# Kernel optimization log

Measured on AMD Instinct MI355X. Metric: run time of the kernel, lower is better.

The kernel has to match this reference:

```python
import jax, jax.numpy as jnp
import numpy as np

B, T, I, H, G = 64, 512, 512, 512, 5  # batch, seq, input, hidden, gates (f,i,o,u,k)


def setup_inputs() -> dict:
    key = jax.random.key(0)
    ks = jax.random.split(key, 9)
    s_in = 1.0 / np.sqrt(I)
    s_h = 1.0 / np.sqrt(H)
    inp = {"x": jax.random.normal(ks[0], (B, T, I), dtype=jnp.float32)}
    # stacked Linear weights, torch layout [out, in]: y = x @ W.T + b
    inp["Wx_f"] = jax.random.uniform(ks[1], (G, H, I), jnp.float32, -s_in, s_in)
    inp["bx_f"] = jax.random.uniform(ks[2], (G, H), jnp.float32, -s_in, s_in)
    inp["Wh_f"] = jax.random.uniform(ks[3], (G, H, H), jnp.float32, -s_h, s_h)
    inp["bh_f"] = jax.random.uniform(ks[4], (G, H), jnp.float32, -s_h, s_h)
    inp["Wx_b"] = jax.random.uniform(ks[5], (G, H, I), jnp.float32, -s_in, s_in)
    inp["bx_b"] = jax.random.uniform(ks[6], (G, H), jnp.float32, -s_in, s_in)
    inp["Wh_b"] = jax.random.uniform(ks[7], (G, H, H), jnp.float32, -s_h, s_h)
    inp["bh_b"] = jax.random.uniform(ks[8], (G, H), jnp.float32, -s_h, s_h)
    return inp


def _run_direction(x, Wx, bx, Wh, bh):
    b, t, _ = x.shape
    h_dim = Wx.shape[1]
    # Precompute all input projections once: [T, B, G, H]
    xp = jnp.einsum('bti,ghi->tbgh', x, Wx) + bx

    def step(carry, xp_t):
        h, k, kp = carry
        g = xp_t + jnp.einsum('bi,goi->bgo', h, Wh) + bh  # [B, G, H]
        f = jax.nn.sigmoid(g[:, 0])
        i = jax.nn.sigmoid(g[:, 1])
        o = jax.nn.sigmoid(g[:, 2])
        u = jax.nn.sigmoid(g[:, 3])
        kp_new = u * jnp.tanh(g[:, 4]) + (1.0 - u) * kp
        k_new = f * k + i * kp_new
        h_new = o * jnp.tanh(k_new)
        return (h_new, k_new, kp_new), h_new

    z = jnp.zeros((b, h_dim), x.dtype)
    _, hs = jax.lax.scan(step, (z, z, z), xp)  # hs: [T, B, H]
    return jnp.transpose(hs, (1, 0, 2))  # [B, T, H]


def reference(x, Wx_f, bx_f, Wh_f, bh_f, Wx_b, bx_b, Wh_b, bh_b):
    out_f = _run_direction(x, Wx_f, bx_f, Wh_f, bh_f)
    out_b = _run_direction(x[:, ::-1], Wx_b, bx_b, Wh_b, bh_b)[:, ::-1]
    # dropout_rate=0.0 / eval mode -> Dropout is identity
    return jnp.concatenate([out_f, out_b], axis=2)  # [B, T, 2H]
```

## Files before the change

kernel.cpp:

```cpp
#include <hip/hip_runtime.h>
#include <hip/hip_bf16.h>

#define B_   64
#define T_   512
#define I_   512
#define H_   512
#define G_   5
#define NROW 2560
#define KD   512

typedef __attribute__((ext_vector_type(8))) __bf16 bf16x8;
typedef __attribute__((ext_vector_type(4))) float  f32x4;
typedef __attribute__((ext_vector_type(2))) unsigned long long u64x2;
typedef unsigned long long u64;

#define MFMA16(A, Bf, C) __builtin_amdgcn_mfma_f32_16x16x32_bf16(A, Bf, C, 0, 0, 0)

__device__ __forceinline__ unsigned short f2bf(float f) {
  unsigned u = __builtin_bit_cast(unsigned, f);
  u = (u + 0x7fffu + ((u >> 16) & 1u)) >> 16;
  return (unsigned short)u;
}
__device__ __forceinline__ float bf2f(unsigned short s) {
  unsigned u = ((unsigned)s) << 16;
  return __builtin_bit_cast(float, u);
}
__device__ __forceinline__ float sigm(float x) { return 1.f / (1.f + __expf(-x)); }
__device__ __forceinline__ float tanh_fast(float x) {
  return 1.f - 2.f / (__expf(2.f * x) + 1.f);
}
__device__ __forceinline__ u64 al64(const u64* p) {
  return __hip_atomic_load(p, __ATOMIC_RELAXED, __HIP_MEMORY_SCOPE_AGENT);
}
__device__ __forceinline__ void as64(u64* p, u64 v) {
  __hip_atomic_store(p, v, __ATOMIC_RELAXED, __HIP_MEMORY_SCOPE_AGENT);
}
__device__ __forceinline__ unsigned al32(const unsigned* p) {
  return __hip_atomic_load(p, __ATOMIC_RELAXED, __HIP_MEMORY_SCOPE_AGENT);
}
__device__ __forceinline__ void st32(unsigned* p, unsigned v) {
  __hip_atomic_store(p, v, __ATOMIC_RELAXED, __HIP_MEMORY_SCOPE_AGENT);
}

#define OFF_XP   ((size_t)0)
#define OFF_XB   ((size_t)335544320)
#define OFF_W2X  ((size_t)369098752)
#define OFF_W2H  ((size_t)374341632)
#define OFF_BIAS ((size_t)379584512)
#define OFF_HB   ((size_t)379604992)
#define OFF_BAR  ((size_t)379867136)
#define WS_NEED  ((size_t)379871232)

__global__ void k_sentinel(float* out, int n) {
  int i = blockIdx.x * 256 + threadIdx.x;
  if (i < n) out[i] = 10000.0f;
}

__global__ void k_cvt_weights(const float* __restrict__ Wx_f, const float* __restrict__ Wh_f,
                              const float* __restrict__ Wx_b, const float* __restrict__ Wh_b,
                              const float* __restrict__ bx_f, const float* __restrict__ bh_f,
                              const float* __restrict__ bx_b, const float* __restrict__ bh_b,
                              unsigned short* __restrict__ W2x, unsigned short* __restrict__ W2h,
                              float* __restrict__ bias2) {
  int idx = blockIdx.x * 256 + threadIdx.x;
  int dir = idx / (NROW * KD);
  int r   = idx % (NROW * KD);
  W2x[idx] = f2bf(dir ? Wx_b[r] : Wx_f[r]);
  W2h[idx] = f2bf(dir ? Wh_b[r] : Wh_f[r]);
  if (idx < 2 * NROW) {
    int d2 = idx / NROW, n = idx % NROW;
    bias2[idx] = d2 ? (bx_b[n] + bh_b[n]) : (bx_f[n] + bh_f[n]);
  }
}

__global__ void k_cvt_x(const float* __restrict__ x, unsigned short* __restrict__ xb) {
  int idx = blockIdx.x * 256 + threadIdx.x;
  xb[idx] = f2bf(x[idx]);
}

__global__ void k_zero_h(unsigned short* __restrict__ hb, unsigned* __restrict__ bar) {
  int idx = blockIdx.x * 256 + threadIdx.x;
  hb[idx] = 0;
  if (idx < 1024) bar[idx] = 0;
}

__global__ __launch_bounds__(256) void k_gemm_xp(
    const unsigned short* __restrict__ W2x,
    const unsigned short* __restrict__ xb,
    const float* __restrict__ bias2,
    unsigned short* __restrict__ xp)
{
  const int tid = threadIdx.x;
  const int lane = tid & 63, wv = tid >> 6;
  int bz = blockIdx.x;
  const int dir = bz / (20 * 256); bz %= (20 * 256);
  const int nblk = bz / 256, mblk = bz % 256;
  const int n0 = nblk * 128, m0 = mblk * 128;
  const int l15 = lane & 15, l4 = lane >> 4;
  const int nh = wv >> 1, mh = wv & 1;

  __shared__ unsigned short Al[128 * 72];
  __shared__ unsigned short Bl[128 * 72];

  const unsigned short* Wd = W2x + (size_t)dir * NROW * KD;

  f32x4 acc[4][4];
  f32x4 zz = {0.f, 0.f, 0.f, 0.f};
#pragma unroll
  for (int i = 0; i < 4; ++i)
#pragma unroll
    for (int j = 0; j < 4; ++j) acc[i][j] = zz;

  for (int k0 = 0; k0 < KD; k0 += 64) {
#pragma unroll
    for (int j = 0; j < 4; ++j) {
      int sg = j * 256 + tid;
      int row = sg >> 3, ko = (sg & 7) * 8;
      bf16x8 va = *(const bf16x8*)(Wd + (size_t)(n0 + row) * KD + k0 + ko);
      *(bf16x8*)(Al + row * 72 + ko) = va;
      int m = m0 + row;
      int ss = m >> 6, b = m & 63;
      int trow = dir ? (T_ - 1 - ss) : ss;
      bf16x8 vb = *(const bf16x8*)(xb + ((size_t)b * T_ + trow) * I_ + k0 + ko);
      *(bf16x8*)(Bl + row * 72 + ko) = vb;
    }
    __syncthreads();
#pragma unroll
    for (int kk = 0; kk < 2; ++kk) {
      bf16x8 af[4], bfr[4];
#pragma unroll
      for (int f = 0; f < 4; ++f) {
        af[f]  = *(const bf16x8*)(Al + (nh * 64 + f * 16 + l15) * 72 + kk * 32 + l4 * 8);
        bfr[f] = *(const bf16x8*)(Bl + (mh * 64 + f * 16 + l15) * 72 + kk * 32 + l4 * 8);
      }
#pragma unroll
      for (int fi = 0; fi < 4; ++fi)
#pragma unroll
        for (int fj = 0; fj < 4; ++fj)
          acc[fi][fj] = MFMA16(af[fi], bfr[fj], acc[fi][fj]);
    }
    __syncthreads();
  }

#pragma unroll
  for (int fi = 0; fi < 4; ++fi) {
#pragma unroll
    for (int fj = 0; fj < 4; ++fj) {
#pragma unroll
      for (int r = 0; r < 4; ++r) {
        int n = n0 + nh * 64 + fi * 16 + l4 * 4 + r;
        int m = m0 + mh * 64 + fj * 16 + l15;
        int ss = m >> 6, b = m & 63;
        float v = acc[fi][fj][r] + bias2[dir * NROW + n];
        xp[(((size_t)dir * T_ + ss) * NROW + n) * 64 + b] = f2bf(v);
      }
    }
  }
}

#define GSTEP(CUR, NXT, NT, NP)                                            \
  {                                                                        \
    _Pragma("unroll")                                                      \
    for (int ks = 0; ks < 16; ++ks)                                        \
      NXT[ks] = *(const bf16x8*)(w_lds + ((NP)*16 + l15) * 520 + ks * 32 + l4 * 8); \
    _Pragma("unroll")                                                      \
    for (int ks = 0; ks < 16; ++ks) {                                      \
      u64x2 t2 = {lo[ks], hi[ks]};                                         \
      bf16x8 a = __builtin_bit_cast(bf16x8, t2);                           \
      acc[NT] = MFMA16(a, CUR[ks], acc[NT]);                               \
    }                                                                      \
  }

__global__ __launch_bounds__(128, 1) void k_recurrent(
    const unsigned short* __restrict__ W2h,
    const unsigned short* __restrict__ xp,
    unsigned short* __restrict__ hbuf,
    float* __restrict__ out,
    unsigned* __restrict__ bar)
{
  const int tid = threadIdx.x;
  const int lane = tid & 63, w = tid >> 6;
  const int bid = blockIdx.x;
  const int dir = bid & 1, bhalf = (bid >> 1) & 1, ublk = bid >> 2;
  const int l15 = lane & 15, l4 = lane >> 4;

  __shared__ unsigned short w_lds[80 * 520];
  __shared__ float          g_sh[2][16 * 84];
  __shared__ unsigned short x_sh[2][80 * 18];

  for (int it = 0; it < 40; ++it) {
    int seg = it * 128 + tid;
    int r = seg >> 6, c8 = seg & 63;
    const unsigned short* src =
        W2h + ((size_t)dir * NROW + (r >> 4) * H_ + ublk * 16 + (r & 15)) * KD + c8 * 8;
    *(bf16x8*)(w_lds + r * 520 + c8 * 8) = *(const bf16x8*)src;
  }
  __syncthreads();

  float* gl = g_sh[w];
  unsigned short* xl = x_sh[w];

  const unsigned short* xpd = xp + (size_t)dir * T_ * NROW * 64;
  const int xoff = bhalf * 16 + w * 8;
  const int batch0 = bhalf * 32 + w * 16;

  unsigned* fl = bar + (dir * 2 + bhalf) * 64;
  const int myflag = ublk * 2 + w;

  const unsigned short* hc = hbuf + (size_t)dir * B_ * H_;
  unsigned short*       hn = hbuf + (size_t)(2 + dir) * B_ * H_;

  const int bl = lane >> 2, uq = (lane & 3) * 4;
  float kst[4] = {0.f, 0.f, 0.f, 0.f}, kp[4] = {0.f, 0.f, 0.f, 0.f};

  unsigned xr[10];
  auto ld_xp = [&](int s) {
    const unsigned* xb32 = (const unsigned*)(xpd + (size_t)s * NROW * 64);
#pragma unroll
    for (int j = 0; j < 10; ++j) {
      int id = j * 64 + lane;
      int r = id >> 3, c = id & 7;
      xr[j] = xb32[((size_t)(r >> 4) * H_ + ublk * 16 + (r & 15)) * 32 + xoff + c];
    }
  };
  ld_xp(0);

  f32x4 zz = {0.f, 0.f, 0.f, 0.f};
  bf16x8 wfA[16], wfB[16];
#pragma unroll
  for (int ks = 0; ks < 16; ++ks)
    wfA[ks] = *(const bf16x8*)(w_lds + l15 * 520 + ks * 32 + l4 * 8);

  auto body = [&](int s, bf16x8 (&cw)[16], bf16x8 (&nw)[16]) {
    if (s) {
      __builtin_amdgcn_sched_barrier(0);
      unsigned tgt = (unsigned)s;
      for (;;) {
        unsigned v = al32(fl + (lane & 31) * 2 + w);
        if (!__any(v < tgt)) break;
        __builtin_amdgcn_s_sleep(1);
      }
      __builtin_amdgcn_sched_barrier(0);
    }

#pragma unroll
    for (int j = 0; j < 10; ++j) {
      int id = j * 64 + lane;
      int r = id >> 3, c = id & 7;
      *(unsigned*)(xl + r * 18 + c * 2) = xr[j];
    }

    const u64* hq = (const u64*)hc;
    u64 lo[16], hi[16];
#pragma unroll
    for (int ks = 0; ks < 16; ++ks) {
      size_t ci = (size_t)(batch0 + l15) * 128 + ks * 8 + l4 * 2;
      lo[ks] = al64(hq + ci);
      hi[ks] = al64(hq + ci + 1);
    }

    f32x4 acc[5] = {zz, zz, zz, zz, zz};
    GSTEP(cw, nw, 0, 1)
    GSTEP(nw, cw, 1, 2)
    GSTEP(cw, nw, 2, 3)
    GSTEP(nw, cw, 3, 4)
    GSTEP(cw, nw, 4, 0)

#pragma unroll
    for (int Nt = 0; Nt < 5; ++Nt)
#pragma unroll
      for (int rr = 0; rr < 4; ++rr)
        gl[(l4 * 4 + rr) * 84 + Nt * 16 + l15] = acc[Nt][rr];
    asm volatile("s_waitcnt lgkmcnt(0)" ::: "memory");
    __builtin_amdgcn_sched_barrier(0);

    float hv[4];
#pragma unroll
    for (int j = 0; j < 4; ++j) {
      int u = uq + j;
      float g0 = gl[bl * 84 + 0 * 16 + u] + bf2f(xl[(0 * 16 + u) * 18 + bl]);
      float g1 = gl[bl * 84 + 1 * 16 + u] + bf2f(xl[(1 * 16 + u) * 18 + bl]);
      float g2 = gl[bl * 84 + 2 * 16 + u] + bf2f(xl[(2 * 16 + u) * 18 + bl]);
      float g3 = gl[bl * 84 + 3 * 16 + u] + bf2f(xl[(3 * 16 + u) * 18 + bl]);
      float g4 = gl[bl * 84 + 4 * 16 + u] + bf2f(xl[(4 * 16 + u) * 18 + bl]);
      float ff = sigm(g0), ii = sigm(g1), oo = sigm(g2), uu = sigm(g3), tk = tanh_fast(g4);
      kp[j]  = uu * tk + (1.f - uu) * kp[j];
      kst[j] = ff * kst[j] + ii * kp[j];
      hv[j]  = oo * tanh_fast(kst[j]);
    }

    u64 hw = (u64)f2bf(hv[0]) | ((u64)f2bf(hv[1]) << 16) |
             ((u64)f2bf(hv[2]) << 32) | ((u64)f2bf(hv[3]) << 48);
    as64((u64*)hn + (size_t)(batch0 + bl) * 128 + (ublk * 16 + uq) / 4, hw);

    int tout = dir ? (T_ - 1 - s) : s;
    float4 o4 = {hv[0], hv[1], hv[2], hv[3]};
    if (s + 1 < T_) {
      asm volatile("s_waitcnt vmcnt(0)" ::: "memory");
      st32(&fl[myflag], (unsigned)(s + 1));
      *(float4*)&out[((size_t)(batch0 + bl) * T_ + tout) * (2 * H_) +
                     dir * H_ + ublk * 16 + uq] = o4;
      ld_xp(s + 1);
    } else {
      *(float4*)&out[((size_t)(batch0 + bl) * T_ + tout) * (2 * H_) +
                     dir * H_ + ublk * 16 + uq] = o4;
    }

    const unsigned short* tp = hc; hc = hn; hn = (unsigned short*)tp;
  };

  for (int s = 0; s < T_; s += 2) {
    body(s,     wfA, wfB);
    body(s + 1, wfB, wfA);
  }
}

extern "C" void kernel_launch(void* const* d_in, const int* in_sizes, int n_in,
                              void* d_out, int out_size, void* d_ws, size_t ws_size,
                              hipStream_t stream) {
  const float* x    = (const float*)d_in[0];
  const float* Wx_f = (const float*)d_in[1];
  const float* bx_f = (const float*)d_in[2];
  const float* Wh_f = (const float*)d_in[3];
  const float* bh_f = (const float*)d_in[4];
  const float* Wx_b = (const float*)d_in[5];
  const float* bx_b = (const float*)d_in[6];
  const float* Wh_b = (const float*)d_in[7];
  const float* bh_b = (const float*)d_in[8];
  float* out = (float*)d_out;

  if (ws_size < WS_NEED) {
    k_sentinel<<<(out_size + 255) / 256, 256, 0, stream>>>(out, out_size);
    return;
  }

  char* ws = (char*)d_ws;
  unsigned short* xp    = (unsigned short*)(ws + OFF_XP);
  unsigned short* xb    = (unsigned short*)(ws + OFF_XB);
  unsigned short* W2x   = (unsigned short*)(ws + OFF_W2X);
  unsigned short* W2h   = (unsigned short*)(ws + OFF_W2H);
  float*          bias2 = (float*)(ws + OFF_BIAS);
  unsigned short* hbuf  = (unsigned short*)(ws + OFF_HB);
  unsigned*       bar   = (unsigned*)(ws + OFF_BAR);

  k_cvt_weights<<<(2 * NROW * KD) / 256, 256, 0, stream>>>(
      Wx_f, Wh_f, Wx_b, Wh_b, bx_f, bh_f, bx_b, bh_b, W2x, W2h, bias2);
  k_cvt_x<<<(B_ * T_ * I_) / 256, 256, 0, stream>>>(x, xb);
  k_zero_h<<<(2 * 2 * B_ * H_) / 256, 256, 0, stream>>>(hbuf, bar);
  k_gemm_xp<<<2 * 20 * 256, 256, 0, stream>>>(W2x, xb, bias2, xp);
  k_recurrent<<<128, 128, 0, stream>>>(W2h, xp, hbuf, out, bar);
}
```

Measured before the change: 2.553 ms.

## Group recurrent workgroups by XCD and sync via XCD-local L2 flags

The recurrent kernel now launches 256 single-wave workgroups instead of 128 two-wave ones. Each workgroup reads its XCD id and takes a rank within that XCD, so each of the 8 (direction, batch-quarter) domains runs entirely on one XCD. Hidden-state exchange and step flags then go through per-domain buffers with sc0 loads and stores, aiming to keep the per-step handoff inside the local L2 instead of going to device-coherent memory. A mirrored device-scope copy of h and the flags serves as a fallback if the placement is uneven or the spin times out. The cost is double writes of h and flags, an extra startup barrier, and reliance on workgroups being spread evenly across XCDs.

```diff
diff --git a/kernel.cpp b/kernel.cpp
--- a/kernel.cpp
+++ b/kernel.cpp
@@ -49,7 +49,8 @@
 #define OFF_BIAS ((size_t)379584512)
 #define OFF_HB   ((size_t)379604992)
 #define OFF_BAR  ((size_t)379867136)
-#define WS_NEED  ((size_t)379871232)
+#define OFF_HMIR ((size_t)379871232)
+#define WS_NEED  ((size_t)380133376)
 
 __global__ void k_sentinel(float* out, int n) {
   int i = blockIdx.x * 256 + threadIdx.x;
@@ -78,9 +79,11 @@
   xb[idx] = f2bf(x[idx]);
 }
 
-__global__ void k_zero_h(unsigned short* __restrict__ hb, unsigned* __restrict__ bar) {
+__global__ void k_zero_h(unsigned* __restrict__ h2, unsigned* __restrict__ hm,
+                         unsigned* __restrict__ bar) {
   int idx = blockIdx.x * 256 + threadIdx.x;
-  hb[idx] = 0;
+  h2[idx] = 0;
+  hm[idx] = 0;
   if (idx < 1024) bar[idx] = 0;
 }
 
@@ -164,63 +167,69 @@
     for (int ks = 0; ks < 16; ++ks)                                        \
       NXT[ks] = *(const bf16x8*)(w_lds + ((NP)*16 + l15) * 520 + ks * 32 + l4 * 8); \
     _Pragma("unroll")                                                      \
-    for (int ks = 0; ks < 16; ++ks) {                                      \
-      u64x2 t2 = {lo[ks], hi[ks]};                                         \
-      bf16x8 a = __builtin_bit_cast(bf16x8, t2);                           \
-      acc[NT] = MFMA16(a, CUR[ks], acc[NT]);                               \
-    }                                                                      \
-  }
-
-__global__ __launch_bounds__(128, 1) void k_recurrent(
+    for (int ks = 0; ks < 16; ++ks)                                        \
+      acc[NT] = MFMA16(ha[ks], CUR[ks], acc[NT]);                          \
+  }
+
+__global__ __launch_bounds__(64, 1) void k_recurrent(
     const unsigned short* __restrict__ W2h,
     const unsigned short* __restrict__ xp,
-    unsigned short* __restrict__ hbuf,
+    unsigned short* __restrict__ hb2,
+    unsigned short* __restrict__ hbm,
     float* __restrict__ out,
     unsigned* __restrict__ bar)
 {
-  const int tid = threadIdx.x;
-  const int lane = tid & 63, w = tid >> 6;
-  const int bid = blockIdx.x;
-  const int dir = bid & 1, bhalf = (bid >> 1) & 1, ublk = bid >> 2;
+  const int lane = threadIdx.x;
   const int l15 = lane & 15, l4 = lane >> 4;
 
   __shared__ unsigned short w_lds[80 * 520];
-  __shared__ float          g_sh[2][16 * 84];
-  __shared__ unsigned short x_sh[2][80 * 18];
-
-  for (int it = 0; it < 40; ++it) {
-    int seg = it * 128 + tid;
+  __shared__ float          gl[16 * 84];
+  __shared__ unsigned short xl[80 * 18];
+
+  unsigned xcd;
+  asm("s_getreg_b32 %0, hwreg(HW_REG_XCC_ID, 0, 4)" : "=s"(xcd));
+  xcd &= 7;
+  unsigned rank = 0;
+  if (lane == 0) rank = atomicAdd(&bar[512 + xcd], 1u);
+  rank = (unsigned)__shfl((int)rank, 0);
+  if (lane == 0) atomicAdd(&bar[520], 1u);
+  while (al32(&bar[520]) < 256u) __builtin_amdgcn_s_sleep(2);
+  bool good = true;
+#pragma unroll
+  for (int x = 0; x < 8; ++x) good = good && (al32(&bar[512 + x]) == 32u);
+
+  int dom, rk;
+  bool l3;
+  if (good && rank < 32u) { dom = (int)xcd; rk = (int)rank; l3 = false; }
+  else                    { dom = blockIdx.x >> 5; rk = blockIdx.x & 31; l3 = true; }
+
+  const int dir = dom >> 2, bq = dom & 3;
+
+  for (int it = 0; it < 80; ++it) {
+    int seg = it * 64 + lane;
     int r = seg >> 6, c8 = seg & 63;
     const unsigned short* src =
-        W2h + ((size_t)dir * NROW + (r >> 4) * H_ + ublk * 16 + (r & 15)) * KD + c8 * 8;
+        W2h + ((size_t)dir * NROW + (r >> 4) * H_ + rk * 16 + (r & 15)) * KD + c8 * 8;
     *(bf16x8*)(w_lds + r * 520 + c8 * 8) = *(const bf16x8*)src;
   }
-  __syncthreads();
-
-  float* gl = g_sh[w];
-  unsigned short* xl = x_sh[w];
 
   const unsigned short* xpd = xp + (size_t)dir * T_ * NROW * 64;
-  const int xoff = bhalf * 16 + w * 8;
-  const int batch0 = bhalf * 32 + w * 16;
-
-  unsigned* fl = bar + (dir * 2 + bhalf) * 64;
-  const int myflag = ublk * 2 + w;
-
-  const unsigned short* hc = hbuf + (size_t)dir * B_ * H_;
-  unsigned short*       hn = hbuf + (size_t)(2 + dir) * B_ * H_;
+  unsigned short* h2d = hb2 + (size_t)dom * 16384;
+  unsigned short* hmd = hbm + (size_t)dom * 16384;
+  unsigned* fl2 = bar + dom * 32;
+  unsigned* flm = bar + 256 + dom * 32;
 
   const int bl = lane >> 2, uq = (lane & 3) * 4;
   float kst[4] = {0.f, 0.f, 0.f, 0.f}, kp[4] = {0.f, 0.f, 0.f, 0.f};
 
   unsigned xr[10];
   auto ld_xp = [&](int s) {
-    const unsigned* xb32 = (const unsigned*)(xpd + (size_t)s * NROW * 64);
+    const unsigned* x32 = (const unsigned*)(xpd + (size_t)s * NROW * 64);
 #pragma unroll
     for (int j = 0; j < 10; ++j) {
       int id = j * 64 + lane;
-      int r = id >> 3, c = id & 7;
-      xr[j] = xb32[((size_t)(r >> 4) * H_ + ublk * 16 + (r & 15)) * 32 + xoff + c];
+      int rl = id >> 3, c = id & 7;
+      xr[j] = x32[((size_t)(rl >> 4) * H_ + rk * 16 + (rl & 15)) * 32 + bq * 8 + c];
     }
   };
   ld_xp(0);
@@ -235,28 +244,54 @@
     if (s) {
       __builtin_amdgcn_sched_barrier(0);
       unsigned tgt = (unsigned)s;
-      for (;;) {
-        unsigned v = al32(fl + (lane & 31) * 2 + w);
-        if (!__any(v < tgt)) break;
-        __builtin_amdgcn_s_sleep(1);
+      if (!l3) {
+        int spins = 0;
+        for (;;) {
+          unsigned v;
+          asm volatile("global_load_dword %0, %1, off sc0\n\ts_waitcnt vmcnt(0)"
+                       : "=v"(v) : "v"(fl2 + (lane & 31)) : "memory");
+          if (!__any(v < tgt)) break;
+          if (++spins > 16384) { l3 = true; break; }
+          __builtin_amdgcn_s_sleep(1);
+        }
+      }
+      if (l3) {
+        for (;;) {
+          unsigned v = al32(flm + (lane & 31));
+          if (!__any(v < tgt)) break;
+          __builtin_amdgcn_s_sleep(1);
+        }
       }
       __builtin_amdgcn_sched_barrier(0);
+    }
+
+    bf16x8 ha[16];
+    {
+      const unsigned short* hq =
+          (l3 ? hmd : h2d) + (s & 1) * 8192 + l15 * 512 + l4 * 8;
+      if (!l3) {
+#pragma unroll
+        for (int ks = 0; ks < 16; ++ks)
+          asm volatile("global_load_dwordx4 %0, %1, off sc0"
+                       : "=v"(ha[ks]) : "v"(hq + ks * 32));
+        asm volatile("s_waitcnt vmcnt(0)" ::: "memory");
+        __builtin_amdgcn_sched_barrier(0);
+      } else {
+#pragma unroll
+        for (int ks = 0; ks < 16; ++ks) {
+          u64 lo = al64((const u64*)(hq + ks * 32));
+          u64 hi = al64((const u64*)(hq + ks * 32) + 1);
+          u64x2 t2 = {lo, hi};
+          ha[ks] = __builtin_bit_cast(bf16x8, t2);
+        }
+      }
     }
 
 #pragma unroll
     for (int j = 0; j < 10; ++j) {
       int id = j * 64 + lane;
-      int r = id >> 3, c = id & 7;
-      *(unsigned*)(xl + r * 18 + c * 2) = xr[j];
-    }
-
-    const u64* hq = (const u64*)hc;
-    u64 lo[16], hi[16];
-#pragma unroll
-    for (int ks = 0; ks < 16; ++ks) {
-      size_t ci = (size_t)(batch0 + l15) * 128 + ks * 8 + l4 * 2;
-      lo[ks] = al64(hq + ci);
-      hi[ks] = al64(hq + ci + 1);
+      int rl = id >> 3, c = id & 7;
+      *(unsigned*)(xl + rl * 18 + c * 2) = xr[j];
     }
 
     f32x4 acc[5] = {zz, zz, zz, zz, zz};
@@ -291,22 +326,30 @@
 
     u64 hw = (u64)f2bf(hv[0]) | ((u64)f2bf(hv[1]) << 16) |
              ((u64)f2bf(hv[2]) << 32) | ((u64)f2bf(hv[3]) << 48);
-    as64((u64*)hn + (size_t)(batch0 + bl) * 128 + (ublk * 16 + uq) / 4, hw);
+    {
+      size_t off = (size_t)((s + 1) & 1) * 8192 + bl * 512 + rk * 16 + uq;
+      asm volatile("global_store_dwordx2 %0, %1, off"
+                   :: "v"(h2d + off), "v"(hw) : "memory");
+      as64((u64*)(hmd + off), hw);
+    }
 
     int tout = dir ? (T_ - 1 - s) : s;
     float4 o4 = {hv[0], hv[1], hv[2], hv[3]};
     if (s + 1 < T_) {
       asm volatile("s_waitcnt vmcnt(0)" ::: "memory");
-      st32(&fl[myflag], (unsigned)(s + 1));
-      *(float4*)&out[((size_t)(batch0 + bl) * T_ + tout) * (2 * H_) +
-                     dir * H_ + ublk * 16 + uq] = o4;
+      if (lane == 0) {
+        unsigned nf = (unsigned)(s + 1);
+        asm volatile("global_store_dword %0, %1, off"
+                     :: "v"(fl2 + rk), "v"(nf) : "memory");
+        st32(flm + rk, nf);
+      }
+      *(float4*)&out[((size_t)(bq * 16 + bl) * T_ + tout) * (2 * H_) +
+                     dir * H_ + rk * 16 + uq] = o4;
       ld_xp(s + 1);
     } else {
-      *(float4*)&out[((size_t)(batch0 + bl) * T_ + tout) * (2 * H_) +
-                     dir * H_ + ublk * 16 + uq] = o4;
-    }
-
-    const unsigned short* tp = hc; hc = hn; hn = (unsigned short*)tp;
+      *(float4*)&out[((size_t)(bq * 16 + bl) * T_ + tout) * (2 * H_) +
+                     dir * H_ + rk * 16 + uq] = o4;
+    }
   };
 
   for (int s = 0; s < T_; s += 2) {
@@ -340,13 +383,14 @@
   unsigned short* W2x   = (unsigned short*)(ws + OFF_W2X);
   unsigned short* W2h   = (unsigned short*)(ws + OFF_W2H);
   float*          bias2 = (float*)(ws + OFF_BIAS);
-  unsigned short* hbuf  = (unsigned short*)(ws + OFF_HB);
+  unsigned short* hb2   = (unsigned short*)(ws + OFF_HB);
   unsigned*       bar   = (unsigned*)(ws + OFF_BAR);
+  unsigned short* hbm   = (unsigned short*)(ws + OFF_HMIR);
 
   k_cvt_weights<<<(2 * NROW * KD) / 256, 256, 0, stream>>>(
       Wx_f, Wh_f, Wx_b, Wh_b, bx_f, bh_f, bx_b, bh_b, W2x, W2h, bias2);
   k_cvt_x<<<(B_ * T_ * I_) / 256, 256, 0, stream>>>(x, xb);
-  k_zero_h<<<(2 * 2 * B_ * H_) / 256, 256, 0, stream>>>(hbuf, bar);
+  k_zero_h<<<256, 256, 0, stream>>>((unsigned*)hb2, (unsigned*)hbm, bar);
   k_gemm_xp<<<2 * 20 * 256, 256, 0, stream>>>(W2x, xb, bias2, xp);
-  k_recurrent<<<128, 128, 0, stream>>>(W2h, xp, hbuf, out, bar);
-}
+  k_recurrent<<<256, 64, 0, stream>>>(W2h, xp, hb2, hbm, out, bar);
+}
```

Result: slower. 3.840 ms (+50.4%).

## Halve recurrent grid; each wave processes two batch sets per step to hide sync latency

Applied to the files above, without the earlier changes.

The recurrent kernel now launches 64 blocks instead of 128. Each wave handles two 16-batch sets in sequence within every timestep, with separate cell state, prefetched projections and barrier flags for each set. The aim is to overlap one set's barrier wait and global latency with the other set's compute, and to reduce the number of blocks taking part in each cross-block flag barrier. In exchange, each block does twice the serial work per step, and the per-set flag layout uses 32 blocks per group.

```diff
diff --git a/kernel.cpp b/kernel.cpp
--- a/kernel.cpp
+++ b/kernel.cpp
@@ -181,7 +181,7 @@
   const int tid = threadIdx.x;
   const int lane = tid & 63, w = tid >> 6;
   const int bid = blockIdx.x;
-  const int dir = bid & 1, bhalf = (bid >> 1) & 1, ublk = bid >> 2;
+  const int dir = bid & 1, ublk = bid >> 1;
   const int l15 = lane & 15, l4 = lane >> 4;
 
   __shared__ unsigned short w_lds[80 * 520];
@@ -201,29 +201,27 @@
   unsigned short* xl = x_sh[w];
 
   const unsigned short* xpd = xp + (size_t)dir * T_ * NROW * 64;
-  const int xoff = bhalf * 16 + w * 8;
-  const int batch0 = bhalf * 32 + w * 16;
-
-  unsigned* fl = bar + (dir * 2 + bhalf) * 64;
-  const int myflag = ublk * 2 + w;
+  const int setA = 2 * w, setB = 2 * w + 1;
 
   const unsigned short* hc = hbuf + (size_t)dir * B_ * H_;
   unsigned short*       hn = hbuf + (size_t)(2 + dir) * B_ * H_;
 
   const int bl = lane >> 2, uq = (lane & 3) * 4;
-  float kst[4] = {0.f, 0.f, 0.f, 0.f}, kp[4] = {0.f, 0.f, 0.f, 0.f};
-
-  unsigned xr[10];
-  auto ld_xp = [&](int s) {
+  float kstA[4] = {0.f, 0.f, 0.f, 0.f}, kpA[4] = {0.f, 0.f, 0.f, 0.f};
+  float kstB[4] = {0.f, 0.f, 0.f, 0.f}, kpB[4] = {0.f, 0.f, 0.f, 0.f};
+
+  unsigned xrA[10], xrB[10];
+  auto ld_xp = [&](int s, int set, unsigned (&xr)[10]) {
     const unsigned* xb32 = (const unsigned*)(xpd + (size_t)s * NROW * 64);
 #pragma unroll
     for (int j = 0; j < 10; ++j) {
       int id = j * 64 + lane;
       int r = id >> 3, c = id & 7;
-      xr[j] = xb32[((size_t)(r >> 4) * H_ + ublk * 16 + (r & 15)) * 32 + xoff + c];
+      xr[j] = xb32[((size_t)(r >> 4) * H_ + ublk * 16 + (r & 15)) * 32 + set * 8 + c];
     }
   };
-  ld_xp(0);
+  ld_xp(0, setA, xrA);
+  ld_xp(0, setB, xrB);
 
   f32x4 zz = {0.f, 0.f, 0.f, 0.f};
   bf16x8 wfA[16], wfB[16];
@@ -231,12 +229,17 @@
   for (int ks = 0; ks < 16; ++ks)
     wfA[ks] = *(const bf16x8*)(w_lds + l15 * 520 + ks * 32 + l4 * 8);
 
-  auto body = [&](int s, bf16x8 (&cw)[16], bf16x8 (&nw)[16]) {
+  auto body = [&](int s, int set, unsigned (&xr)[10],
+                  float (&kst)[4], float (&kp)[4],
+                  bf16x8 (&cw)[16], bf16x8 (&nw)[16]) {
+    unsigned* fl = bar + (dir * 4 + set) * 32;
+    const int batch0 = set * 16;
+
     if (s) {
       __builtin_amdgcn_sched_barrier(0);
       unsigned tgt = (unsigned)s;
       for (;;) {
-        unsigned v = al32(fl + (lane & 31) * 2 + w);
+        unsigned v = al32(fl + (lane & 31));
         if (!__any(v < tgt)) break;
         __builtin_amdgcn_s_sleep(1);
       }
@@ -297,21 +300,20 @@
     float4 o4 = {hv[0], hv[1], hv[2], hv[3]};
     if (s + 1 < T_) {
       asm volatile("s_waitcnt vmcnt(0)" ::: "memory");
-      st32(&fl[myflag], (unsigned)(s + 1));
+      if (lane == 0) st32(&fl[ublk], (unsigned)(s + 1));
       *(float4*)&out[((size_t)(batch0 + bl) * T_ + tout) * (2 * H_) +
                      dir * H_ + ublk * 16 + uq] = o4;
-      ld_xp(s + 1);
+      ld_xp(s + 1, set, xr);
     } else {
       *(float4*)&out[((size_t)(batch0 + bl) * T_ + tout) * (2 * H_) +
                      dir * H_ + ublk * 16 + uq] = o4;
     }
-
+  };
+
+  for (int s = 0; s < T_; ++s) {
+    body(s, setA, xrA, kstA, kpA, wfA, wfB);
+    body(s, setB, xrB, kstB, kpB, wfB, wfA);
     const unsigned short* tp = hc; hc = hn; hn = (unsigned short*)tp;
-  };
-
-  for (int s = 0; s < T_; s += 2) {
-    body(s,     wfA, wfB);
-    body(s + 1, wfB, wfA);
   }
 }
 
@@ -348,5 +350,5 @@
   k_cvt_x<<<(B_ * T_ * I_) / 256, 256, 0, stream>>>(x, xb);
   k_zero_h<<<(2 * 2 * B_ * H_) / 256, 256, 0, stream>>>(hbuf, bar);
   k_gemm_xp<<<2 * 20 * 256, 256, 0, stream>>>(W2x, xb, bias2, xp);
-  k_recurrent<<<128, 128, 0, stream>>>(W2h, xp, hbuf, out, bar);
-}
+  k_recurrent<<<64, 128, 0, stream>>>(W2h, xp, hbuf, out, bar);
+}
```

Result: slower. 4.538 ms (+77.8%).
